# Kernel optimization log

Measured on AMD Instinct MI355X. Metric: run time of the kernel, lower is better.

The kernel has to match this reference:

```python
import jax, jax.numpy as jnp
import numpy as np

BN_EPS = 1e-5
RMS_EPS = 1e-6
LA_EPS = 0.0005


def _conv_bn(x, w, gamma, beta):
    """1x1 conv (no bias) + BatchNorm2d with batch stats (training mode)."""
    y = jnp.einsum('oc,bchw->bohw', w, x)
    mean = y.mean(axis=(0, 2, 3), keepdims=True)
    var = y.var(axis=(0, 2, 3), keepdims=True)
    return gamma[None, :, None, None] * (y - mean) * jax.lax.rsqrt(var + BN_EPS) + beta[None, :, None, None]


def setup_inputs() -> dict:
    key = jax.random.key(0)
    k0, k1, k2 = jax.random.split(key, 3)
    dim, d = 512, 512  # d = make_divisible(dim / attn_reduce, 8) with attn_reduce=1
    x = jax.random.normal(k0, (8, dim, 64, 64), jnp.float32)
    qkvg_w = jax.random.normal(k1, (4 * d, dim), jnp.float32) * (dim ** -0.5)
    qkvg_gamma = jnp.ones((4 * d,), jnp.float32)
    qkvg_beta = jnp.zeros((4 * d,), jnp.float32)
    attn_norm_w = jnp.ones((d,), jnp.float32)
    proj_w = jax.random.normal(k2, (dim, d), jnp.float32) * (d ** -0.5)
    proj_gamma = jnp.ones((dim,), jnp.float32)
    proj_beta = jnp.zeros((dim,), jnp.float32)
    return {"x": x, "qkvg_w": qkvg_w, "qkvg_gamma": qkvg_gamma, "qkvg_beta": qkvg_beta,
            "attn_norm_w": attn_norm_w, "proj_w": proj_w, "proj_gamma": proj_gamma,
            "proj_beta": proj_beta}


def reference(x, qkvg_w, qkvg_gamma, qkvg_beta, attn_norm_w, proj_w, proj_gamma, proj_beta):
    B, C, H, W = x.shape
    y = _conv_bn(x, qkvg_w, qkvg_gamma, qkvg_beta).reshape(B, -1, H * W)  # (B, 4d, N)
    q, k, v, g = jnp.split(y, 4, axis=1)  # each (B, d, N)

    # LA branch: kernel feature map + linear-associativity (use_linear True since N > d)
    q = jax.nn.sigmoid(q)
    k = jax.nn.sigmoid(k)
    n = q.shape[-1]
    scale = n ** -0.5  # kT.shape[-2] ** -0.5
    # z = kT.mean(-2, keepdims) @ q + eps  -> (B, 1, N), computed on UNscaled k
    z = jnp.einsum('bd,bdn->bn', k.mean(axis=-1), q)[:, None, :] + LA_EPS
    # attn = (v*s) @ (kT*s) @ q ; contract over N first: (B,d,d), then over d
    vk = jnp.einsum('bdn,ben->bde', v * scale, k * scale)  # (B, d, d)
    attn = jnp.einsum('bde,ben->bdn', vk, q) / z  # (B, d, N)

    # RMSNorm over channel dim d
    o = attn * jax.lax.rsqrt(jnp.mean(attn * attn, axis=1, keepdims=True) + RMS_EPS)
    o = o * attn_norm_w[None, :, None]

    # gate + output projection
    o = o * jax.nn.silu(g)
    o = o.reshape(B, -1, H, W)
    return _conv_bn(o, proj_w, proj_gamma, proj_beta)
```

## Files before the change

kernel.cpp:

```cpp
#include <hip/hip_runtime.h>
#include <hip/hip_bf16.h>
#include <math.h>

typedef unsigned short u16;
typedef __attribute__((ext_vector_type(8))) short frag8;
typedef __attribute__((ext_vector_type(4))) float f32x4;
typedef __attribute__((ext_vector_type(8))) unsigned short us8;
typedef __attribute__((ext_vector_type(4))) unsigned short us4;

#define B_ 8
#define C_ 512
#define D_ 512
#define N_ 4096

__device__ __forceinline__ float b2f(u16 u){ union { unsigned int i; float f; } v; v.i = ((unsigned int)u) << 16; return v.f; }
__device__ __forceinline__ u16 f2b(float f){ union { float f; unsigned int i; } v; v.f = f; unsigned int x = v.i; return (u16)((x + 0x7fffu + ((x >> 16) & 1u)) >> 16); }
__device__ __forceinline__ float sigm(float x){ return 1.0f / (1.0f + __expf(-x)); }

__device__ __forceinline__ void gl2l(const u16* g, u16* l){
    __builtin_amdgcn_global_load_lds((const __attribute__((address_space(1))) void*)g,
                                     (__attribute__((address_space(3))) void*)l, 16, 0, 0);
}

__device__ __forceinline__ us8 load_x8(const void* __restrict__ x, int fl, size_t off){
    if (fl){
        const float* p = (const float*)x + off;
        f32x4 a = *(const f32x4*)p;
        f32x4 b = *(const f32x4*)(p + 4);
        us8 o;
        #pragma unroll
        for (int j = 0; j < 4; ++j){ o[j] = f2b(a[j]); o[4 + j] = f2b(b[j]); }
        return o;
    }
    return *(const us8*)((const u16*)x + off);
}

__global__ __launch_bounds__(256) void k_detect(const unsigned int* __restrict__ x, int* __restrict__ flag){
    int tid = threadIdx.x;
    unsigned int w = x[tid];
    int e = (int)((w >> 7) & 0xFFu);
    int in = (e >= 100 && e <= 140) ? 1 : 0;
    __shared__ int sm[4];
    for (int off = 32; off > 0; off >>= 1) in += __shfl_down(in, off);
    if ((tid & 63) == 0) sm[tid >> 6] = in;
    __syncthreads();
    if (tid == 0) *flag = ((sm[0] + sm[1] + sm[2] + sm[3]) < 128) ? 1 : 0;
}

__global__ __launch_bounds__(256) void k_convert(const void* __restrict__ src, u16* __restrict__ dst,
                                                 int n, const int* __restrict__ flag){
    int i = (blockIdx.x * 256 + threadIdx.x) * 8;
    if (i >= n) return;
    *(us8*)(dst + i) = load_x8(src, *flag, (size_t)i);
}

__global__ __launch_bounds__(256) void k_xpose(const void* __restrict__ x, const int* __restrict__ flag,
                                               u16* __restrict__ xT){
    __shared__ __attribute__((aligned(16))) u16 T[64][72];
    int rt = blockIdx.y;
    int b = rt >> 3, c0 = (rt & 7) * 64;
    int n0 = blockIdx.x * 64;
    int tid = threadIdx.x, fl = *flag;
    int row = tid >> 2, cg = (tid & 3) * 16;
    size_t base = ((size_t)b * C_ + c0 + row) * N_ + n0 + cg;
    us8 v0 = load_x8(x, fl, base);
    us8 v1 = load_x8(x, fl, base + 8);
    #pragma unroll
    for (int j = 0; j < 8; ++j){ T[cg + j][row] = v0[j]; T[cg + 8 + j][row] = v1[j]; }
    __syncthreads();
    int col = tid >> 2, rg = (tid & 3) * 16;
    us8 o0 = *(const us8*)&T[col][rg];
    us8 o1 = *(const us8*)&T[col][rg + 8];
    u16* dst = xT + ((size_t)b * N_ + n0 + col) * C_ + c0 + rg;
    *(us8*)dst = o0;
    *(us8*)(dst + 8) = o1;
}

__global__ __launch_bounds__(256) void k_xmean(const void* __restrict__ x, const int* __restrict__ flag,
                                               float* __restrict__ mx){
    int k = blockIdx.x, tid = threadIdx.x, fl = *flag;
    float sum = 0.f;
    for (int b = 0; b < B_; ++b){
        size_t base = ((size_t)b * C_ + k) * N_;
        for (int i = tid * 8; i < N_; i += 2048){
            us8 v = load_x8(x, fl, base + i);
            #pragma unroll
            for (int j = 0; j < 8; ++j) sum += b2f(v[j]);
        }
    }
    __shared__ float sm[4];
    for (int off = 32; off > 0; off >>= 1) sum += __shfl_down(sum, off);
    if ((tid & 63) == 0) sm[tid >> 6] = sum;
    __syncthreads();
    if (tid == 0) mx[k] = (sm[0] + sm[1] + sm[2] + sm[3]) * (1.0f / 32768.0f);
}

__global__ __launch_bounds__(256) void k_gram_split(const void* __restrict__ x, const int* __restrict__ flag,
                                                    float* __restrict__ Gf){
    __shared__ __attribute__((aligned(16))) u16 As[64][40];
    __shared__ __attribute__((aligned(16))) u16 Bs[64][40];
    int k0 = blockIdx.y * 64, kp0 = blockIdx.x * 64;
    int s = blockIdx.z;
    int b = s >> 2, nbase = (s & 3) * 1024;
    int tid = threadIdx.x, row = tid >> 2, cg = (tid & 3) * 8;
    int w = tid >> 6, l = tid & 63, lr = l & 15, q = l >> 4;
    int fl = *flag;
    f32x4 acc[4] = {};
    size_t abase = ((size_t)b * C_ + k0 + row) * N_ + nbase + cg;
    size_t bbase = ((size_t)b * C_ + kp0 + row) * N_ + nbase + cg;
    for (int n0 = 0; n0 < 1024; n0 += 32){
        *(us8*)&As[row][cg] = load_x8(x, fl, abase + n0);
        *(us8*)&Bs[row][cg] = load_x8(x, fl, bbase + n0);
        __syncthreads();
        frag8 af = *(const frag8*)&As[w * 16 + lr][q * 8];
        #pragma unroll
        for (int t4 = 0; t4 < 4; ++t4){
            frag8 bfv = *(const frag8*)&Bs[t4 * 16 + lr][q * 8];
            acc[t4] = __builtin_amdgcn_mfma_f32_16x16x32_bf16(af, bfv, acc[t4], 0, 0, 0);
        }
        __syncthreads();
    }
    #pragma unroll
    for (int t4 = 0; t4 < 4; ++t4)
        #pragma unroll
        for (int r = 0; r < 4; ++r)
            atomicAdd(&Gf[(size_t)(k0 + w * 16 + q * 4 + r) * C_ + kp0 + t4 * 16 + lr], acc[t4][r]);
}

__global__ __launch_bounds__(256) void k_gram_fin(const float* __restrict__ Gf, u16* __restrict__ Gb){
    int i = blockIdx.x * 256 + threadIdx.x;
    Gb[i] = f2b(Gf[i] * (1.0f / 32768.0f));
}

__global__ __launch_bounds__(256) void k_wg(const u16* __restrict__ wc, const u16* __restrict__ Gb, float* __restrict__ T){
    __shared__ __attribute__((aligned(16))) u16 As[64][40];
    __shared__ __attribute__((aligned(16))) u16 Bs[64][40];
    int o0 = blockIdx.y * 64, kp0 = blockIdx.x * 64;
    int tid = threadIdx.x, row = tid >> 2, cg = (tid & 3) * 8;
    const u16* ap = wc + (size_t)(o0 + row) * C_ + cg;
    const u16* bp = Gb + (size_t)(kp0 + row) * C_ + cg;
    int w = tid >> 6, l = tid & 63, lr = l & 15, q = l >> 4;
    f32x4 acc[4] = {};
    for (int k0 = 0; k0 < 512; k0 += 32){
        *(us8*)&As[row][cg] = *(const us8*)(ap + k0);
        *(us8*)&Bs[row][cg] = *(const us8*)(bp + k0);
        __syncthreads();
        frag8 af = *(const frag8*)&As[w * 16 + lr][q * 8];
        #pragma unroll
        for (int t4 = 0; t4 < 4; ++t4){
            frag8 bfv = *(const frag8*)&Bs[t4 * 16 + lr][q * 8];
            acc[t4] = __builtin_amdgcn_mfma_f32_16x16x32_bf16(af, bfv, acc[t4], 0, 0, 0);
        }
        __syncthreads();
    }
    #pragma unroll
    for (int t4 = 0; t4 < 4; ++t4)
        #pragma unroll
        for (int r = 0; r < 4; ++r)
            T[(size_t)(o0 + w * 16 + q * 4 + r) * C_ + kp0 + t4 * 16 + lr] = acc[t4][r];
}

__global__ __launch_bounds__(256) void k_bn1fin(const float* __restrict__ T, const u16* __restrict__ wc,
                                                const float* __restrict__ mx, const u16* __restrict__ g1,
                                                const u16* __restrict__ b1, float* __restrict__ s1,
                                                float* __restrict__ t1){
    int o = blockIdx.x, tid = threadIdx.x;
    float e2 = 0.f, mn = 0.f;
    for (int k = tid; k < 512; k += 256){
        float wv = b2f(wc[(size_t)o * C_ + k]);
        e2 += T[(size_t)o * C_ + k] * wv;
        mn += wv * mx[k];
    }
    __shared__ float sm[8];
    for (int off = 32; off > 0; off >>= 1){ e2 += __shfl_down(e2, off); mn += __shfl_down(mn, off); }
    int w = tid >> 6;
    if ((tid & 63) == 0){ sm[w] = e2; sm[4 + w] = mn; }
    __syncthreads();
    if (tid == 0){
        float E2 = sm[0] + sm[1] + sm[2] + sm[3];
        float M  = sm[4] + sm[5] + sm[6] + sm[7];
        float var = E2 - M * M;
        float inv = rsqrtf(var + 1e-5f);
        float sc = b2f(g1[o]) * inv;
        s1[o] = sc;
        t1[o] = b2f(b1[o]) - M * sc;
    }
}

template<int PHASE>
__global__ __launch_bounds__(256) void k_gemm_act(const u16* __restrict__ wc, const u16* __restrict__ xT,
                                                  const float* __restrict__ s1, const float* __restrict__ t1,
                                                  u16* __restrict__ dst){
    __shared__ __attribute__((aligned(16))) u16 As[128 * 32];
    __shared__ __attribute__((aligned(16))) u16 Bs[128 * 32];
    int b = blockIdx.z, n0 = blockIdx.x * 128, my = blockIdx.y;
    int c0 = (PHASE == 1) ? (512 + my * 128) : ((my < 4) ? my * 128 : 1536 + (my - 4) * 128);
    int tid = threadIdx.x, w = tid >> 6, l = tid & 63, lr = l & 15, q = l >> 4;
    int wr = w & 1, wcn = w >> 1;
    int srow = l >> 2, scol = (l & 3) * 8;
    const u16* ap = wc + (size_t)(c0 + w * 16 + srow) * C_ + scol;
    const u16* bp = xT + ((size_t)b * N_ + n0 + w * 16 + srow) * C_ + scol;
    u16* la = As + w * 512;
    u16* lb = Bs + w * 512;
    f32x4 acc[4][4] = {};
    for (int k0 = 0; k0 < 512; k0 += 32){
        gl2l(ap + k0, la);
        gl2l(ap + k0 + (size_t)64 * C_, la + 2048);
        gl2l(bp + k0, lb);
        gl2l(bp + k0 + (size_t)64 * C_, lb + 2048);
        __syncthreads();
        frag8 af[4], bf[4];
        #pragma unroll
        for (int i = 0; i < 4; ++i){
            af[i] = *(const frag8*)&As[(wr * 64 + i * 16 + lr) * 32 + q * 8];
            bf[i] = *(const frag8*)&Bs[(wcn * 64 + i * 16 + lr) * 32 + q * 8];
        }
        #pragma unroll
        for (int mi = 0; mi < 4; ++mi)
            #pragma unroll
            for (int ni = 0; ni < 4; ++ni)
                acc[mi][ni] = __builtin_amdgcn_mfma_f32_16x16x32_bf16(af[mi], bf[ni], acc[mi][ni], 0, 0, 0);
        __syncthreads();
    }
    #pragma unroll
    for (int mi = 0; mi < 4; ++mi){
        int cb = c0 + wr * 64 + mi * 16 + q * 4;
        #pragma unroll
        for (int ni = 0; ni < 4; ++ni){
            int n = n0 + wcn * 64 + ni * 16 + lr;
            us4 o4;
            #pragma unroll
            for (int r = 0; r < 4; ++r){
                int c = cb + r;
                float ybn = acc[mi][ni][r] * s1[c] + t1[c];
                float ov = (c < 1024) ? sigm(ybn) : ((c < 1536) ? ybn : ybn * sigm(ybn));
                if (PHASE == 1)
                    dst[((size_t)b * 1024 + (c - 512)) * N_ + n] = f2b(ov);
                else
                    o4[r] = f2b(ov);
            }
            if (PHASE == 2){
                int col = (cb < 512) ? cb : (cb - 1024);
                *(us4*)(dst + ((size_t)b * N_ + n) * 1024 + col) = o4;
            }
        }
    }
}

__global__ __launch_bounds__(256) void k_vk(const u16* __restrict__ kv, u16* __restrict__ vk){
    __shared__ __attribute__((aligned(16))) u16 As[64][40];
    __shared__ __attribute__((aligned(16))) u16 Bs[64][40];
    int b = blockIdx.z, d0 = blockIdx.y * 64, e0 = blockIdx.x * 64;
    int tid = threadIdx.x, row = tid >> 2, cg = (tid & 3) * 8;
    const u16* vp = kv + ((size_t)b * 1024 + 512 + d0 + row) * N_ + cg;
    const u16* kp = kv + ((size_t)b * 1024 + e0 + row) * N_ + cg;
    int w = tid >> 6, l = tid & 63, lr = l & 15, q = l >> 4;
    f32x4 acc[4] = {};
    for (int n0 = 0; n0 < N_; n0 += 32){
        *(us8*)&As[row][cg] = *(const us8*)(vp + n0);
        *(us8*)&Bs[row][cg] = *(const us8*)(kp + n0);
        __syncthreads();
        frag8 af = *(const frag8*)&As[w * 16 + lr][q * 8];
        #pragma unroll
        for (int t4 = 0; t4 < 4; ++t4){
            frag8 bfv = *(const frag8*)&Bs[t4 * 16 + lr][q * 8];
            acc[t4] = __builtin_amdgcn_mfma_f32_16x16x32_bf16(af, bfv, acc[t4], 0, 0, 0);
        }
        __syncthreads();
    }
    #pragma unroll
    for (int t4 = 0; t4 < 4; ++t4)
        #pragma unroll
        for (int r = 0; r < 4; ++r)
            vk[((size_t)b * D_ + d0 + w * 16 + q * 4 + r) * D_ + e0 + t4 * 16 + lr] = f2b(acc[t4][r] * (1.0f / 4096.0f));
}

__global__ __launch_bounds__(256) void k_kmean(const u16* __restrict__ kv, u16* __restrict__ kmean){
    int b = blockIdx.y, d = blockIdx.x, tid = threadIdx.x;
    const u16* p = kv + ((size_t)b * 1024 + d) * N_;
    float sum = 0.f;
    for (int i = tid * 8; i < N_; i += 2048){
        us8 v = *(const us8*)(p + i);
        #pragma unroll
        for (int j = 0; j < 8; ++j) sum += b2f(v[j]);
    }
    __shared__ float sm[4];
    for (int off = 32; off > 0; off >>= 1) sum += __shfl_down(sum, off);
    if ((tid & 63) == 0) sm[tid >> 6] = sum;
    __syncthreads();
    if (tid == 0) kmean[b * D_ + d] = f2b((sm[0] + sm[1] + sm[2] + sm[3]) * (1.0f / 4096.0f));
}

__global__ __launch_bounds__(256) void k_attn(const u16* __restrict__ qg, const u16* __restrict__ vk,
                                              const u16* __restrict__ kmean, const u16* __restrict__ anw,
                                              u16* __restrict__ og){
    __shared__ __attribute__((aligned(16))) u16 Xls[32][520];
    __shared__ float sred[4][32];
    int b = blockIdx.y, n0 = blockIdx.x * 32, tid = threadIdx.x;
    int wv = tid >> 6, l = tid & 63, lr = l & 15, q = l >> 4;
    const u16* qb = qg + ((size_t)b * N_ + n0) * 1024;
    #pragma unroll
    for (int it = 0; it < 8; ++it){
        int g = it * 256 + tid;
        int row = g >> 6, col = (g & 63) * 8;
        *(us8*)&Xls[row][col] = *(const us8*)(qb + (size_t)row * 1024 + col);
    }
    __syncthreads();
    const u16* vkb = vk + (size_t)b * D_ * D_ + (size_t)(wv * 128) * D_;
    const u16* kmb = kmean + (size_t)b * D_;
    f32x4 acc[8][2] = {};
    f32x4 accz[2] = {};
    for (int e0 = 0; e0 < 512; e0 += 32){
        frag8 bfv[2];
        #pragma unroll
        for (int nn = 0; nn < 2; ++nn)
            bfv[nn] = *(const frag8*)&Xls[nn * 16 + lr][e0 + q * 8];
        frag8 zf = {};
        if (lr == 0) zf = *(const frag8*)(kmb + e0 + q * 8);
        #pragma unroll
        for (int nn = 0; nn < 2; ++nn)
            accz[nn] = __builtin_amdgcn_mfma_f32_16x16x32_bf16(zf, bfv[nn], accz[nn], 0, 0, 0);
        #pragma unroll
        for (int dd = 0; dd < 8; ++dd){
            frag8 af = *(const frag8*)(vkb + (size_t)(dd * 16 + lr) * D_ + e0 + q * 8);
            #pragma unroll
            for (int nn = 0; nn < 2; ++nn)
                acc[dd][nn] = __builtin_amdgcn_mfma_f32_16x16x32_bf16(af, bfv[nn], acc[dd][nn], 0, 0, 0);
        }
    }
    float rz[2];
    #pragma unroll
    for (int nn = 0; nn < 2; ++nn)
        rz[nn] = 1.0f / (__shfl(accz[nn][0], lr) + 0.0005f);
    float ssq[2] = {0.f, 0.f};
    #pragma unroll
    for (int dd = 0; dd < 8; ++dd)
        #pragma unroll
        for (int nn = 0; nn < 2; ++nn)
            #pragma unroll
            for (int r = 0; r < 4; ++r){
                float a = acc[dd][nn][r] * rz[nn];
                acc[dd][nn][r] = a;
                ssq[nn] += a * a;
            }
    #pragma unroll
    for (int nn = 0; nn < 2; ++nn){
        ssq[nn] += __shfl_xor(ssq[nn], 16);
        ssq[nn] += __shfl_xor(ssq[nn], 32);
    }
    if (l < 16){ sred[wv][l] = ssq[0]; sred[wv][16 + l] = ssq[1]; }
    __syncthreads();
    float rinv[2];
    #pragma unroll
    for (int nn = 0; nn < 2; ++nn){
        float t = sred[0][nn * 16 + lr] + sred[1][nn * 16 + lr] + sred[2][nn * 16 + lr] + sred[3][nn * 16 + lr];
        rinv[nn] = rsqrtf(t * (1.0f / 512.0f) + 1e-6f);
    }
    #pragma unroll
    for (int dd = 0; dd < 8; ++dd){
        int dbase = wv * 128 + dd * 16 + q * 4;
        us4 aw4 = *(const us4*)(anw + dbase);
        #pragma unroll
        for (int nn = 0; nn < 2; ++nn){
            int n = n0 + nn * 16 + lr;
            us4 g4 = *(const us4*)(qb + (size_t)(nn * 16 + lr) * 1024 + 512 + dbase);
            us4 o4;
            #pragma unroll
            for (int r = 0; r < 4; ++r)
                o4[r] = f2b(acc[dd][nn][r] * rinv[nn] * b2f(aw4[r]) * b2f(g4[r]));
            *(us4*)(og + ((size_t)b * N_ + n) * D_ + dbase) = o4;
        }
    }
}

__global__ __launch_bounds__(256) void k_proj(const u16* __restrict__ P, const u16* __restrict__ og, float* __restrict__ po){
    __shared__ __attribute__((aligned(16))) u16 As[128 * 32];
    __shared__ __attribute__((aligned(16))) u16 Bs[128 * 32];
    int b = blockIdx.z, n0 = blockIdx.x * 128, c0 = blockIdx.y * 128;
    int tid = threadIdx.x, w = tid >> 6, l = tid & 63, lr = l & 15, q = l >> 4;
    int wr = w & 1, wcn = w >> 1;
    int srow = l >> 2, scol = (l & 3) * 8;
    const u16* ap = P + (size_t)(c0 + w * 16 + srow) * D_ + scol;
    const u16* bp = og + ((size_t)b * N_ + n0 + w * 16 + srow) * D_ + scol;
    u16* la = As + w * 512;
    u16* lb = Bs + w * 512;
    f32x4 acc[4][4] = {};
    for (int k0 = 0; k0 < 512; k0 += 32){
        gl2l(ap + k0, la);
        gl2l(ap + k0 + (size_t)64 * D_, la + 2048);
        gl2l(bp + k0, lb);
        gl2l(bp + k0 + (size_t)64 * D_, lb + 2048);
        __syncthreads();
        frag8 af[4], bf[4];
        #pragma unroll
        for (int i = 0; i < 4; ++i){
            af[i] = *(const frag8*)&As[(wr * 64 + i * 16 + lr) * 32 + q * 8];
            bf[i] = *(const frag8*)&Bs[(wcn * 64 + i * 16 + lr) * 32 + q * 8];
        }
        #pragma unroll
        for (int mi = 0; mi < 4; ++mi)
            #pragma unroll
            for (int ni = 0; ni < 4; ++ni)
                acc[mi][ni] = __builtin_amdgcn_mfma_f32_16x16x32_bf16(af[mi], bf[ni], acc[mi][ni], 0, 0, 0);
        __syncthreads();
    }
    #pragma unroll
    for (int mi = 0; mi < 4; ++mi){
        int cb = c0 + wr * 64 + mi * 16 + q * 4;
        #pragma unroll
        for (int ni = 0; ni < 4; ++ni){
            int n = n0 + wcn * 64 + ni * 16 + lr;
            #pragma unroll
            for (int r = 0; r < 4; ++r)
                po[((size_t)b * C_ + cb + r) * N_ + n] = acc[mi][ni][r];
        }
    }
}

__global__ __launch_bounds__(256) void k_bnstats(const float* __restrict__ y, const u16* __restrict__ gamma,
                                                 const u16* __restrict__ beta, float* __restrict__ s,
                                                 float* __restrict__ t){
    int ch = blockIdx.x, tid = threadIdx.x;
    float sum = 0.f, ss = 0.f;
    for (int b = 0; b < B_; ++b){
        const float* p = y + ((size_t)b * C_ + ch) * N_;
        for (int i = tid * 4; i < N_; i += 1024){
            f32x4 v = *(const f32x4*)(p + i);
            #pragma unroll
            for (int j = 0; j < 4; ++j){ sum += v[j]; ss += v[j] * v[j]; }
        }
    }
    __shared__ float sm[8];
    for (int off = 32; off > 0; off >>= 1){ sum += __shfl_down(sum, off); ss += __shfl_down(ss, off); }
    int w = tid >> 6;
    if ((tid & 63) == 0){ sm[w] = sum; sm[4 + w] = ss; }
    __syncthreads();
    if (tid == 0){
        float S = sm[0] + sm[1] + sm[2] + sm[3];
        float Q = sm[4] + sm[5] + sm[6] + sm[7];
        float mean = S / 32768.f;
        float var = Q / 32768.f - mean * mean;
        float inv = rsqrtf(var + 1e-5f);
        float sc = b2f(gamma[ch]) * inv;
        s[ch] = sc;
        t[ch] = b2f(beta[ch]) - mean * sc;
    }
}

__global__ __launch_bounds__(256) void k_bnapply(float* __restrict__ po, const float* __restrict__ s,
                                                 const float* __restrict__ t){
    size_t idx = ((size_t)blockIdx.x * 256 + threadIdx.x) * 8;
    int c = (int)((idx >> 12) & 511);
    float sc = s[c], tc = t[c];
    f32x4 a = *(const f32x4*)(po + idx);
    f32x4 b = *(const f32x4*)(po + idx + 4);
    #pragma unroll
    for (int j = 0; j < 4; ++j){ a[j] = a[j] * sc + tc; b[j] = b[j] * sc + tc; }
    *(f32x4*)(po + idx) = a;
    *(f32x4*)(po + idx + 4) = b;
}

extern "C" void kernel_launch(void* const* d_in, const int* in_sizes, int n_in,
                              void* d_out, int out_size, void* d_ws, size_t ws_size,
                              hipStream_t stream){
    float* out = (float*)d_out;
    char* ws = (char*)d_ws;

    int*   flag  = (int*)ws;
    float* s1    = (float*)(ws + 4096);
    float* t1    = (float*)(ws + 12288);
    float* s2    = (float*)(ws + 20480);
    float* t2    = (float*)(ws + 22528);
    float* mx    = (float*)(ws + 24576);
    u16*   kmean = (u16*)(ws + 28672);
    u16*   g1c   = (u16*)(ws + 36864);
    u16*   b1c   = (u16*)(ws + 40960);
    u16*   anwc  = (u16*)(ws + 45056);
    u16*   g2c   = (u16*)(ws + 46080);
    u16*   b2c   = (u16*)(ws + 47104);
    u16*   wc    = (u16*)(ws + (1ull << 20));
    u16*   pc    = (u16*)(ws + (3ull << 20));
    u16*   Gb    = (u16*)(ws + (3584ull << 10));
    float* T     = (float*)(ws + (4ull << 20));
    u16*   vkall = (u16*)(ws + (8ull << 20));
    u16*   kv    = (u16*)(ws + (12ull << 20));
    u16*   og    = (u16*)(ws + (76ull << 20));
    u16*   xT    = (u16*)(ws + (76ull << 20));
    float* Gf    = (float*)(ws + (108ull << 20));

    k_detect<<<1, 256, 0, stream>>>((const unsigned int*)d_in[0], flag);
    k_convert<<<512, 256, 0, stream>>>(d_in[1], wc, 1048576, flag);
    k_convert<<<1, 256, 0, stream>>>(d_in[2], g1c, 2048, flag);
    k_convert<<<1, 256, 0, stream>>>(d_in[3], b1c, 2048, flag);
    k_convert<<<1, 256, 0, stream>>>(d_in[4], anwc, 512, flag);
    k_convert<<<128, 256, 0, stream>>>(d_in[5], pc, 262144, flag);
    k_convert<<<1, 256, 0, stream>>>(d_in[6], g2c, 512, flag);
    k_convert<<<1, 256, 0, stream>>>(d_in[7], b2c, 512, flag);

    k_xpose<<<dim3(64, 64), 256, 0, stream>>>(d_in[0], flag, xT);

    hipMemsetAsync(Gf, 0, C_ * C_ * sizeof(float), stream);
    k_xmean<<<512, 256, 0, stream>>>(d_in[0], flag, mx);
    k_gram_split<<<dim3(8, 8, 32), 256, 0, stream>>>(d_in[0], flag, Gf);
    k_gram_fin<<<1024, 256, 0, stream>>>(Gf, Gb);
    k_wg<<<dim3(8, 32), 256, 0, stream>>>(wc, Gb, T);
    k_bn1fin<<<2048, 256, 0, stream>>>(T, wc, mx, g1c, b1c, s1, t1);

    k_gemm_act<1><<<dim3(32, 8, 8), 256, 0, stream>>>(wc, xT, s1, t1, kv);
    k_vk<<<dim3(8, 8, 8), 256, 0, stream>>>(kv, vkall);
    k_kmean<<<dim3(512, 8), 256, 0, stream>>>(kv, kmean);

    k_gemm_act<2><<<dim3(32, 8, 8), 256, 0, stream>>>(wc, xT, s1, t1, kv);
    k_attn<<<dim3(128, 8), 256, 0, stream>>>(kv, vkall, kmean, anwc, og);

    k_proj<<<dim3(32, 4, 8), 256, 0, stream>>>(pc, og, out);
    k_bnstats<<<512, 256, 0, stream>>>(out, g2c, b2c, s2, t2);
    k_bnapply<<<8192, 256, 0, stream>>>(out, s2, t2);
}
```

Baseline: 626.8 us.

## Enlarge Gram and vk GEMM tiles and stage loads via global_load_lds

The Gram kernel now reads a pre-converted bf16 copy of x, filled by a new conversion pass, instead of converting on the fly. It uses 128x128 tiles with a 4x4 MFMA grid per wave. The vk kernel moves to 64x128 tiles. Both kernels load global memory straight into LDS with global_load_lds, which cuts staging instructions and raises data reuse per tile. The cost is an extra full pass over x (64MB read, 32MB write), more accumulator registers, and unpadded LDS rows that may cause bank conflicts.

After: 616.7 us. No clear change (-1.6%).

```diff
diff --git a/kernel.cpp b/kernel.cpp
--- a/kernel.cpp
+++ b/kernel.cpp
@@ -95,36 +95,47 @@
     if (tid == 0) mx[k] = (sm[0] + sm[1] + sm[2] + sm[3]) * (1.0f / 32768.0f);
 }
 
-__global__ __launch_bounds__(256) void k_gram_split(const void* __restrict__ x, const int* __restrict__ flag,
-                                                    float* __restrict__ Gf){
-    __shared__ __attribute__((aligned(16))) u16 As[64][40];
-    __shared__ __attribute__((aligned(16))) u16 Bs[64][40];
-    int k0 = blockIdx.y * 64, kp0 = blockIdx.x * 64;
+__global__ __launch_bounds__(256) void k_gram_split(const u16* __restrict__ xc, float* __restrict__ Gf){
+    __shared__ __attribute__((aligned(16))) u16 As[128 * 32];
+    __shared__ __attribute__((aligned(16))) u16 Bs[128 * 32];
+    int k0 = blockIdx.y * 128, kp0 = blockIdx.x * 128;
     int s = blockIdx.z;
     int b = s >> 2, nbase = (s & 3) * 1024;
-    int tid = threadIdx.x, row = tid >> 2, cg = (tid & 3) * 8;
-    int w = tid >> 6, l = tid & 63, lr = l & 15, q = l >> 4;
-    int fl = *flag;
-    f32x4 acc[4] = {};
-    size_t abase = ((size_t)b * C_ + k0 + row) * N_ + nbase + cg;
-    size_t bbase = ((size_t)b * C_ + kp0 + row) * N_ + nbase + cg;
+    int tid = threadIdx.x, w = tid >> 6, l = tid & 63, lr = l & 15, q = l >> 4;
+    int wr = w & 1, wcn = w >> 1;
+    int srow = l >> 2, scol = (l & 3) * 8;
+    const u16* ap = xc + ((size_t)b * C_ + k0 + w * 16 + srow) * N_ + nbase + scol;
+    const u16* bp = xc + ((size_t)b * C_ + kp0 + w * 16 + srow) * N_ + nbase + scol;
+    u16* la = As + w * 512;
+    u16* lb = Bs + w * 512;
+    f32x4 acc[4][4] = {};
     for (int n0 = 0; n0 < 1024; n0 += 32){
-        *(us8*)&As[row][cg] = load_x8(x, fl, abase + n0);
-        *(us8*)&Bs[row][cg] = load_x8(x, fl, bbase + n0);
-        __syncthreads();
-        frag8 af = *(const frag8*)&As[w * 16 + lr][q * 8];
-        #pragma unroll
-        for (int t4 = 0; t4 < 4; ++t4){
-            frag8 bfv = *(const frag8*)&Bs[t4 * 16 + lr][q * 8];
-            acc[t4] = __builtin_amdgcn_mfma_f32_16x16x32_bf16(af, bfv, acc[t4], 0, 0, 0);
-        }
-        __syncthreads();
-    }
-    #pragma unroll
-    for (int t4 = 0; t4 < 4; ++t4)
-        #pragma unroll
-        for (int r = 0; r < 4; ++r)
-            atomicAdd(&Gf[(size_t)(k0 + w * 16 + q * 4 + r) * C_ + kp0 + t4 * 16 + lr], acc[t4][r]);
+        gl2l(ap + n0, la);
+        gl2l(ap + n0 + (size_t)64 * N_, la + 2048);
+        gl2l(bp + n0, lb);
+        gl2l(bp + n0 + (size_t)64 * N_, lb + 2048);
+        __syncthreads();
+        frag8 af[4], bf[4];
+        #pragma unroll
+        for (int i = 0; i < 4; ++i){
+            af[i] = *(const frag8*)&As[(wr * 64 + i * 16 + lr) * 32 + q * 8];
+            bf[i] = *(const frag8*)&Bs[(wcn * 64 + i * 16 + lr) * 32 + q * 8];
+        }
+        #pragma unroll
+        for (int mi = 0; mi < 4; ++mi)
+            #pragma unroll
+            for (int ni = 0; ni < 4; ++ni)
+                acc[mi][ni] = __builtin_amdgcn_mfma_f32_16x16x32_bf16(af[mi], bf[ni], acc[mi][ni], 0, 0, 0);
+        __syncthreads();
+    }
+    #pragma unroll
+    for (int mi = 0; mi < 4; ++mi)
+        #pragma unroll
+        for (int ni = 0; ni < 4; ++ni)
+            #pragma unroll
+            for (int r = 0; r < 4; ++r)
+                atomicAdd(&Gf[(size_t)(k0 + wr * 64 + mi * 16 + q * 4 + r) * C_ + kp0 + wcn * 64 + ni * 16 + lr],
+                          acc[mi][ni][r]);
 }
 
 __global__ __launch_bounds__(256) void k_gram_fin(const float* __restrict__ Gf, u16* __restrict__ Gb){
@@ -248,31 +259,44 @@
 }
 
 __global__ __launch_bounds__(256) void k_vk(const u16* __restrict__ kv, u16* __restrict__ vk){
-    __shared__ __attribute__((aligned(16))) u16 As[64][40];
-    __shared__ __attribute__((aligned(16))) u16 Bs[64][40];
-    int b = blockIdx.z, d0 = blockIdx.y * 64, e0 = blockIdx.x * 64;
-    int tid = threadIdx.x, row = tid >> 2, cg = (tid & 3) * 8;
-    const u16* vp = kv + ((size_t)b * 1024 + 512 + d0 + row) * N_ + cg;
-    const u16* kp = kv + ((size_t)b * 1024 + e0 + row) * N_ + cg;
-    int w = tid >> 6, l = tid & 63, lr = l & 15, q = l >> 4;
-    f32x4 acc[4] = {};
+    __shared__ __attribute__((aligned(16))) u16 As[64 * 32];
+    __shared__ __attribute__((aligned(16))) u16 Bs[128 * 32];
+    int b = blockIdx.z, d0 = blockIdx.y * 64, e0 = blockIdx.x * 128;
+    int tid = threadIdx.x, w = tid >> 6, l = tid & 63, lr = l & 15, q = l >> 4;
+    int wr = w & 1, wcn = w >> 1;
+    int srow = l >> 2, scol = (l & 3) * 8;
+    const u16* ap = kv + ((size_t)b * 1024 + 512 + d0 + w * 16 + srow) * N_ + scol;
+    const u16* bp = kv + ((size_t)b * 1024 + e0 + w * 32 + srow) * N_ + scol;
+    u16* la = As + w * 512;
+    u16* lb = Bs + w * 1024;
+    f32x4 acc[2][4] = {};
     for (int n0 = 0; n0 < N_; n0 += 32){
-        *(us8*)&As[row][cg] = *(const us8*)(vp + n0);
-        *(us8*)&Bs[row][cg] = *(const us8*)(kp + n0);
-        __syncthreads();
-        frag8 af = *(const frag8*)&As[w * 16 + lr][q * 8];
-        #pragma unroll
-        for (int t4 = 0; t4 < 4; ++t4){
-            frag8 bfv = *(const frag8*)&Bs[t4 * 16 + lr][q * 8];
-            acc[t4] = __builtin_amdgcn_mfma_f32_16x16x32_bf16(af, bfv, acc[t4], 0, 0, 0);
-        }
-        __syncthreads();
-    }
-    #pragma unroll
-    for (int t4 = 0; t4 < 4; ++t4)
-        #pragma unroll
-        for (int r = 0; r < 4; ++r)
-            vk[((size_t)b * D_ + d0 + w * 16 + q * 4 + r) * D_ + e0 + t4 * 16 + lr] = f2b(acc[t4][r] * (1.0f / 4096.0f));
+        gl2l(ap + n0, la);
+        gl2l(bp + n0, lb);
+        gl2l(bp + n0 + (size_t)16 * N_, lb + 512);
+        __syncthreads();
+        frag8 af[2], bf[4];
+        #pragma unroll
+        for (int i = 0; i < 2; ++i)
+            af[i] = *(const frag8*)&As[(wr * 32 + i * 16 + lr) * 32 + q * 8];
+        #pragma unroll
+        for (int i = 0; i < 4; ++i)
+            bf[i] = *(const frag8*)&Bs[(wcn * 64 + i * 16 + lr) * 32 + q * 8];
+        #pragma unroll
+        for (int mi = 0; mi < 2; ++mi)
+            #pragma unroll
+            for (int ni = 0; ni < 4; ++ni)
+                acc[mi][ni] = __builtin_amdgcn_mfma_f32_16x16x32_bf16(af[mi], bf[ni], acc[mi][ni], 0, 0, 0);
+        __syncthreads();
+    }
+    #pragma unroll
+    for (int mi = 0; mi < 2; ++mi)
+        #pragma unroll
+        for (int ni = 0; ni < 4; ++ni)
+            #pragma unroll
+            for (int r = 0; r < 4; ++r)
+                vk[((size_t)b * D_ + d0 + wr * 32 + mi * 16 + q * 4 + r) * D_ + e0 + wcn * 64 + ni * 16 + lr]
+                    = f2b(acc[mi][ni][r] * (1.0f / 4096.0f));
 }
 
 __global__ __launch_bounds__(256) void k_kmean(const u16* __restrict__ kv, u16* __restrict__ kmean){
@@ -484,6 +508,7 @@
     float* T     = (float*)(ws + (4ull << 20));
     u16*   vkall = (u16*)(ws + (8ull << 20));
     u16*   kv    = (u16*)(ws + (12ull << 20));
+    u16*   xc    = (u16*)(ws + (12ull << 20));
     u16*   og    = (u16*)(ws + (76ull << 20));
     u16*   xT    = (u16*)(ws + (76ull << 20));
     float* Gf    = (float*)(ws + (108ull << 20));
@@ -497,17 +522,18 @@
     k_convert<<<1, 256, 0, stream>>>(d_in[6], g2c, 512, flag);
     k_convert<<<1, 256, 0, stream>>>(d_in[7], b2c, 512, flag);
 
+    k_convert<<<8192, 256, 0, stream>>>(d_in[0], xc, 16777216, flag);
     k_xpose<<<dim3(64, 64), 256, 0, stream>>>(d_in[0], flag, xT);
 
     hipMemsetAsync(Gf, 0, C_ * C_ * sizeof(float), stream);
     k_xmean<<<512, 256, 0, stream>>>(d_in[0], flag, mx);
-    k_gram_split<<<dim3(8, 8, 32), 256, 0, stream>>>(d_in[0], flag, Gf);
+    k_gram_split<<<dim3(4, 4, 32), 256, 0, stream>>>(xc, Gf);
     k_gram_fin<<<1024, 256, 0, stream>>>(Gf, Gb);
     k_wg<<<dim3(8, 32), 256, 0, stream>>>(wc, Gb, T);
     k_bn1fin<<<2048, 256, 0, stream>>>(T, wc, mx, g1c, b1c, s1, t1);
 
     k_gemm_act<1><<<dim3(32, 8, 8), 256, 0, stream>>>(wc, xT, s1, t1, kv);
-    k_vk<<<dim3(8, 8, 8), 256, 0, stream>>>(kv, vkall);
+    k_vk<<<dim3(4, 8, 8), 256, 0, stream>>>(kv, vkall);
     k_kmean<<<dim3(512, 8), 256, 0, stream>>>(kv, kmean);
 
     k_gemm_act<2><<<dim3(32, 8, 8), 256, 0, stream>>>(wc, xT, s1, t1, kv);
```
